# Kernel tuning notes

Measured on AMD Instinct MI355X. Metric: run time of the kernel, lower is better.

## Reference

```python
import jax, jax.numpy as jnp
import numpy as np

C = 1024          # channels
RED = 16          # reduction
RC = C // RED     # 64 bottleneck channels
BZ, NUM_PROPS = 4, 256
BP = BZ * NUM_PROPS


def setup_inputs() -> dict:
    key = jax.random.key(0)
    ks = jax.random.split(key, 10)
    x_props = jax.random.normal(ks[0], (BP, C, 7, 7), dtype=jnp.float32)
    x_query = jax.random.normal(ks[1], (BZ, C, 8, 8), dtype=jnp.float32)
    s_conv = 1.0 / np.sqrt(C)   # kaiming-uniform-ish for conv1d 1x1 (fan_in=C)
    s_mlp = 1.0 / np.sqrt(RC)   # Linear fan_in = RC
    pc_w = jax.random.uniform(ks[2], (RC, C), minval=-s_conv, maxval=s_conv)
    pc_b = jax.random.uniform(ks[3], (RC,), minval=-s_conv, maxval=s_conv)
    qc_w = jax.random.uniform(ks[4], (RC, C), minval=-s_conv, maxval=s_conv)
    qc_b = jax.random.uniform(ks[5], (RC,), minval=-s_conv, maxval=s_conv)
    pm_w = jax.random.uniform(ks[6], (C, RC), minval=-s_mlp, maxval=s_mlp)
    pm_b = jax.random.uniform(ks[7], (C,), minval=-s_mlp, maxval=s_mlp)
    qm_w = jax.random.uniform(ks[8], (C, RC), minval=-s_mlp, maxval=s_mlp)
    qm_b = jax.random.uniform(ks[9], (C,), minval=-s_mlp, maxval=s_mlp)
    return {"x_props": x_props, "x_query": x_query,
            "pc_w": pc_w, "pc_b": pc_b, "qc_w": qc_w, "qc_b": qc_b,
            "pm_w": pm_w, "pm_b": pm_b, "qm_w": qm_w, "qm_b": qm_b}


def reference(x_props, x_query, pc_w, pc_b, qc_w, qc_b, pm_w, pm_b, qm_w, qm_b):
    bp, c, hp, wp = x_props.shape
    bz, _, hq, wq = x_query.shape
    n = bp // bz
    L = hp * wp
    # bilinear resize (half-pixel centers == torch align_corners=False)
    r_query = jax.image.resize(x_query, (bz, c, hp, wp), method='bilinear')
    # 1x1 conv bottlenecks (conv1d over flattened spatial dim)
    q_feat = jnp.einsum('rc,bcl->brl', qc_w, r_query.reshape(bz, c, L)) + qc_b[None, :, None]   # [bz, RC, L]
    p_feat = jnp.einsum('rc,bcl->brl', pc_w, x_props.reshape(bp, c, L)) + pc_b[None, :, None]   # [bp, RC, L]
    # similarity contracts spatial dim; query feature shared across props of same image
    p_feat_g = p_feat.reshape(bz, n, -1, L)
    sim = jnp.einsum('bnrl,bsl->bnrs', p_feat_g, q_feat)                                        # [bz, n, RC, RC]
    p_rel = sim.mean(axis=3).reshape(bp, -1)                                                    # [bp, RC]
    q_rel = sim.mean(axis=2).reshape(bp, -1)                                                    # [bp, RC]
    # channel-gate MLPs
    p_att = jax.nn.sigmoid(p_rel @ pm_w.T + pm_b)                                               # [bp, C]
    q_att = jax.nn.sigmoid(q_rel @ qm_w.T + qm_b)                                               # [bp, C]
    # co-excitation
    f_props = x_props * p_att[:, :, None, None]
    xq_rep = jnp.broadcast_to(x_query[:, None], (bz, n, c, hq, wq)).reshape(bp, c, hq, wq)
    f_query = xq_rep * q_att[:, :, None, None]
    return f_props, f_query, p_att.reshape(bp, c, 1, 1)
```

## Files before the change

### kernel.cpp

```cpp
#include <hip/hip_runtime.h>


typedef float v4f __attribute__((ext_vector_type(4)));

#define WQBAR  0
#define WPCBW  320
#define WPCBB  1344
#define WQF    1408
#define WPMBF  14336
#define WQMBF  47104

#define OUT_FP 0
#define OUT_FQ 51380224
#define OUT_PA 118489088

__device__ __forceinline__ float sigmoidf(float v) {
    return 1.0f / (1.0f + __expf(-v));
}
__device__ __forceinline__ unsigned short bf16_rne(float x) {
    unsigned u = __float_as_uint(x);
    return (unsigned short)((u + 0x7FFFu + ((u >> 16) & 1u)) >> 16);
}
__device__ __forceinline__ unsigned div49(unsigned e) {
    return __umulhi(e, 2804876602u) >> 5;
}

__global__ __launch_bounds__(1024) void k_prepall(
    const float* __restrict__ xq, const float* __restrict__ qc_w,
    const float* __restrict__ qc_b, const float* __restrict__ pc_w,
    const float* __restrict__ pc_b, const float* __restrict__ pm_w,
    const float* __restrict__ qm_w, float* __restrict__ ws)
{
    const int blk = blockIdx.x, t = threadIdx.x;
    if (blk < 196) {
        __shared__ float rq[1024];
        __shared__ float qf_s[64];
        const int b = blk / 49, l = blk - b * 49;
        const int wave = t >> 6, lane = t & 63;
        const int i = l / 7, j = l - i * 7;
        float fi = (2 * i + 1) * (1.0f / 14.0f);
        float fj = (2 * j + 1) * (1.0f / 14.0f);
        float wi0 = (1.0f - 0.875f * fi) * (1.0f / 1.125f); float wi1 = 1.0f - wi0;
        float wj0 = (1.0f - 0.875f * fj) * (1.0f / 1.125f); float wj1 = 1.0f - wj0;
        const float* X = xq + ((size_t)(b * 1024 + t) << 6);
        rq[t] = wi0 * (wj0 * X[i * 8 + j]       + wj1 * X[i * 8 + j + 1])
              + wi1 * (wj0 * X[(i + 1) * 8 + j] + wj1 * X[(i + 1) * 8 + j + 1]);
        __syncthreads();
        #pragma unroll
        for (int ii = 0; ii < 4; ++ii) {
            int s = wave * 4 + ii;
            const float* wr = qc_w + s * 1024;
            float part = 0.0f;
            #pragma unroll
            for (int k = 0; k < 16; ++k) part += wr[k * 64 + lane] * rq[k * 64 + lane];
            #pragma unroll
            for (int off = 32; off; off >>= 1) part += __shfl_down(part, off, 64);
            if (lane == 0) {
                float val = part + qc_b[s];
                ws[WQF + b * 3136 + s * 49 + l] = val;
                qf_s[s] = val;
            }
        }
        __syncthreads();
        if (t == 0) {
            float s = 0.0f;
            #pragma unroll
            for (int k = 0; k < 64; ++k) s += qf_s[k];
            ws[WQBAR + b * 49 + l] = s * (1.0f / 64.0f);
        }
    } else if (blk == 196) {
        float s = 0.0f;
        for (int r = 0; r < 64; ++r) s += pc_w[r * 1024 + t];
        ws[WPCBW + t] = s * (1.0f / 64.0f);
        if (t == 0) {
            float sb = 0.0f;
            for (int r = 0; r < 64; ++r) sb += pc_b[r];
            ws[WPCBB] = sb * (1.0f / 64.0f);
        }
    } else {
        int idx = (blk - 197) * 1024 + t;
        int r = (idx & 65535) >> 10, c = idx & 1023;
        float w = (idx < 65536) ? pm_w[c * 64 + r] : qm_w[c * 64 + r];
        unsigned short* dst = (unsigned short*)(ws + (idx < 65536 ? WPMBF : WQMBF));
        dst[idx & 65535] = bf16_rne(w);
    }
}

__global__ __launch_bounds__(256) void k_red(
    const float* __restrict__ x, const float* __restrict__ xq,
    const float* __restrict__ pc_w, const float* __restrict__ pc_b,
    const float* __restrict__ pm_b, const float* __restrict__ qm_b,
    float* __restrict__ ws, float* __restrict__ patt_out,
    float* __restrict__ fquery)
{
    __shared__ float xs[6272];
    __shared__ float y_s[1024];
    __shared__ float pcb_s[1024];
    __shared__ float qbar_s[49];
    __shared__ float sq_s;
    __shared__ float pbar_part[2][49];
    __shared__ float pbar_s[49];
    __shared__ float prel_s[64];
    __shared__ float qrel_s[64];

    const int t = threadIdx.x, wave = t >> 6, lane = t & 63;
    const int p = blockIdx.x, b = p >> 8;

    if (t < 49) qbar_s[t] = ws[WQBAR + b * 49 + t];
    for (int k = t; k < 1024; k += 256) pcb_s[k] = ws[WPCBW + k];
    const float pcbarb = ws[WPCBB];

    const float4* xp4 = (const float4*)(x + (size_t)p * 50176);
    float pbar_acc = 0.0f;

    for (int ch = 0; ch < 8; ++ch) {
        __syncthreads();
        const float4* src = xp4 + ch * 1568;
        float4* xs4 = (float4*)xs;
        for (int k = t; k < 1568; k += 256) xs4[k] = src[k];
        __syncthreads();
        if (ch == 0 && t == 0) {
            float s = 0.0f;
            #pragma unroll
            for (int l = 0; l < 49; ++l) s += qbar_s[l];
            sq_s = s;
        }
        if (wave < 2) {
            int c = wave * 64 + lane;
            const float* row = xs + c * 49;
            float acc = 0.0f;
            #pragma unroll
            for (int l = 0; l < 49; ++l) acc += row[l] * qbar_s[l];
            y_s[ch * 128 + c] = acc;
        } else if (lane < 49) {
            int cw = (wave - 2) * 64;
            const float* base = xs + cw * 49 + lane;
            const float* pw = pcb_s + ch * 128 + cw;
            float a = 0.0f;
            #pragma unroll
            for (int c = 0; c < 64; ++c) a += pw[c] * base[c * 49];
            pbar_acc += a;
        }
    }
    if (wave >= 2 && lane < 49) pbar_part[wave - 2][lane] = pbar_acc;
    __syncthreads();
    if (t < 49) pbar_s[t] = pbar_part[0][t] + pbar_part[1][t] + pcbarb;
    __syncthreads();
    const float sumqbar = sq_s;

    #pragma unroll
    for (int i = 0; i < 16; ++i) {
        int r = wave * 16 + i;
        const float* wr = pc_w + r * 1024;
        float part = 0.0f;
        #pragma unroll
        for (int k = 0; k < 16; ++k) part += wr[k * 64 + lane] * y_s[k * 64 + lane];
        #pragma unroll
        for (int off = 32; off; off >>= 1) part += __shfl_down(part, off, 64);
        if (lane == 0) prel_s[r] = part + pc_b[r] * sumqbar;
    }
    if (t < 64) {
        const float* qfr = ws + WQF + (b * 3136 + t * 49);
        float a = 0.0f;
        #pragma unroll
        for (int l = 0; l < 49; ++l) a += pbar_s[l] * qfr[l];
        qrel_s[t] = a;
    }
    __syncthreads();

    {
        const unsigned* wp = (const unsigned*)(ws + WPMBF);
        const unsigned* wq = (const unsigned*)(ws + WQMBF);
        float4 ap = {0, 0, 0, 0}, aq = {0, 0, 0, 0};
        #pragma unroll
        for (int r = 0; r < 64; ++r) {
            float pr = prel_s[r], qr = qrel_s[r];
            unsigned p01 = wp[r * 512 + 2 * t];
            unsigned p23 = wp[r * 512 + 2 * t + 1];
            ap.x += __uint_as_float(p01 << 16) * pr;
            ap.y += __uint_as_float(p01 & 0xFFFF0000u) * pr;
            ap.z += __uint_as_float(p23 << 16) * pr;
            ap.w += __uint_as_float(p23 & 0xFFFF0000u) * pr;
            unsigned q01 = wq[r * 512 + 2 * t];
            unsigned q23 = wq[r * 512 + 2 * t + 1];
            aq.x += __uint_as_float(q01 << 16) * qr;
            aq.y += __uint_as_float(q01 & 0xFFFF0000u) * qr;
            aq.z += __uint_as_float(q23 << 16) * qr;
            aq.w += __uint_as_float(q23 & 0xFFFF0000u) * qr;
        }
        float4 pb = ((const float4*)pm_b)[t];
        float4 qb = ((const float4*)qm_b)[t];
        float4 po, qo;
        po.x = sigmoidf(ap.x + pb.x); po.y = sigmoidf(ap.y + pb.y);
        po.z = sigmoidf(ap.z + pb.z); po.w = sigmoidf(ap.w + pb.w);
        qo.x = sigmoidf(aq.x + qb.x); qo.y = sigmoidf(aq.y + qb.y);
        qo.z = sigmoidf(aq.z + qb.z); qo.w = sigmoidf(aq.w + qb.w);
        ((float4*)patt_out)[p * 256 + t] = po;
        ((float4*)pcb_s)[t] = qo;
    }
    __syncthreads();

    const v4f* xq4 = (const v4f*)(xq + ((size_t)b << 16));
    v4f* fq4 = (v4f*)(fquery + ((size_t)p << 16));
    #pragma unroll
    for (int i = 0; i < 64; ++i) {
        int k = i * 256 + t;
        float att = pcb_s[k >> 4];
        v4f v = xq4[k];
        __builtin_nontemporal_store(v * att, fq4 + k);
    }
}

__global__ __launch_bounds__(256) void k_scale(
    const float* __restrict__ x, const float* __restrict__ patt,
    float* __restrict__ fprops)
{
    const unsigned N4 = 12845056u;
    const unsigned stride = gridDim.x * blockDim.x;
    for (unsigned i = blockIdx.x * blockDim.x + threadIdx.x; i < N4; i += stride) {
        unsigned e = i * 4u;
        unsigned q = div49(e);
        unsigned m = e - 49u * q;
        float a0 = patt[q];
        float a1 = patt[q + (m >= 46u)];
        v4f v = ((const v4f*)x)[i];
        v4f g;
        g.x = a0;
        g.y = (m >= 48u) ? a1 : a0;
        g.z = (m >= 47u) ? a1 : a0;
        g.w = (m >= 46u) ? a1 : a0;
        __builtin_nontemporal_store(v * g, (v4f*)fprops + i);
    }
}

extern "C" void kernel_launch(void* const* d_in, const int* in_sizes, int n_in,
                              void* d_out, int out_size, void* d_ws, size_t ws_size,
                              hipStream_t stream) {
    const float* x_props = (const float*)d_in[0];
    const float* x_query = (const float*)d_in[1];
    const float* pc_w    = (const float*)d_in[2];
    const float* pc_b    = (const float*)d_in[3];
    const float* qc_w    = (const float*)d_in[4];
    const float* qc_b    = (const float*)d_in[5];
    const float* pm_w    = (const float*)d_in[6];
    const float* pm_b    = (const float*)d_in[7];
    const float* qm_w    = (const float*)d_in[8];
    const float* qm_b    = (const float*)d_in[9];
    float* out = (float*)d_out;
    float* ws  = (float*)d_ws;

    k_prepall<<<325, 1024, 0, stream>>>(x_query, qc_w, qc_b, pc_w, pc_b, pm_w, qm_w, ws);
    k_red<<<1024, 256, 0, stream>>>(x_props, x_query, pc_w, pc_b, pm_b, qm_b, ws,
                                    out + OUT_PA, out + OUT_FQ);
    k_scale<<<4096, 256, 0, stream>>>(x_props, out + OUT_PA, out + OUT_FP);
}
```

Measured before the change: 168.0 us.

## Fuse proposal scaling into per-proposal reduction kernel to reuse x_props

```diff
diff --git a/kernel.cpp b/kernel.cpp
--- a/kernel.cpp
+++ b/kernel.cpp
@@ -86,12 +86,12 @@
     }
 }
 
-__global__ __launch_bounds__(256) void k_red(
+__global__ __launch_bounds__(256) void k_main(
     const float* __restrict__ x, const float* __restrict__ xq,
     const float* __restrict__ pc_w, const float* __restrict__ pc_b,
     const float* __restrict__ pm_b, const float* __restrict__ qm_b,
     float* __restrict__ ws, float* __restrict__ patt_out,
-    float* __restrict__ fquery)
+    float* __restrict__ fprops, float* __restrict__ fquery)
 {
     __shared__ float xs[6272];
     __shared__ float y_s[1024];
@@ -196,40 +196,41 @@
         qo.x = sigmoidf(aq.x + qb.x); qo.y = sigmoidf(aq.y + qb.y);
         qo.z = sigmoidf(aq.z + qb.z); qo.w = sigmoidf(aq.w + qb.w);
         ((float4*)patt_out)[p * 256 + t] = po;
+        __syncthreads();
+        ((float4*)y_s)[t]   = po;
         ((float4*)pcb_s)[t] = qo;
     }
     __syncthreads();
 
-    const v4f* xq4 = (const v4f*)(xq + ((size_t)b << 16));
-    v4f* fq4 = (v4f*)(fquery + ((size_t)p << 16));
-    #pragma unroll
-    for (int i = 0; i < 64; ++i) {
-        int k = i * 256 + t;
-        float att = pcb_s[k >> 4];
-        v4f v = xq4[k];
-        __builtin_nontemporal_store(v * att, fq4 + k);
-    }
-}
-
-__global__ __launch_bounds__(256) void k_scale(
-    const float* __restrict__ x, const float* __restrict__ patt,
-    float* __restrict__ fprops)
-{
-    const unsigned N4 = 12845056u;
-    const unsigned stride = gridDim.x * blockDim.x;
-    for (unsigned i = blockIdx.x * blockDim.x + threadIdx.x; i < N4; i += stride) {
-        unsigned e = i * 4u;
-        unsigned q = div49(e);
-        unsigned m = e - 49u * q;
-        float a0 = patt[q];
-        float a1 = patt[q + (m >= 46u)];
-        v4f v = ((const v4f*)x)[i];
-        v4f g;
-        g.x = a0;
-        g.y = (m >= 48u) ? a1 : a0;
-        g.z = (m >= 47u) ? a1 : a0;
-        g.w = (m >= 46u) ? a1 : a0;
-        __builtin_nontemporal_store(v * g, (v4f*)fprops + i);
+    {
+        const v4f* xg4 = (const v4f*)(x + (size_t)p * 50176);
+        v4f* fp4 = (v4f*)(fprops + (size_t)p * 50176);
+        for (int i = 0; i < 49; ++i) {
+            int k = i * 256 + t;
+            unsigned e = 4u * (unsigned)k;
+            unsigned c0 = div49(e);
+            unsigned m = e - 49u * c0;
+            float a0 = y_s[c0];
+            float a1 = y_s[c0 + (m >= 46u)];
+            v4f v = xg4[k];
+            v4f g;
+            g.x = a0;
+            g.y = (m >= 48u) ? a1 : a0;
+            g.z = (m >= 47u) ? a1 : a0;
+            g.w = (m >= 46u) ? a1 : a0;
+            __builtin_nontemporal_store(v * g, fp4 + k);
+        }
+    }
+
+    {
+        const v4f* xq4 = (const v4f*)(xq + ((size_t)b << 16));
+        v4f* fq4 = (v4f*)(fquery + ((size_t)p << 16));
+        for (int i = 0; i < 64; ++i) {
+            int k = i * 256 + t;
+            float att = pcb_s[k >> 4];
+            v4f v = xq4[k];
+            __builtin_nontemporal_store(v * att, fq4 + k);
+        }
     }
 }
 
@@ -250,7 +251,6 @@
     float* ws  = (float*)d_ws;
 
     k_prepall<<<325, 1024, 0, stream>>>(x_query, qc_w, qc_b, pc_w, pc_b, pm_w, qm_w, ws);
-    k_red<<<1024, 256, 0, stream>>>(x_props, x_query, pc_w, pc_b, pm_b, qm_b, ws,
-                                    out + OUT_PA, out + OUT_FQ);
-    k_scale<<<4096, 256, 0, stream>>>(x_props, out + OUT_PA, out + OUT_FP);
-}
+    k_main<<<1024, 256, 0, stream>>>(x_props, x_query, pc_w, pc_b, pm_b, qm_b, ws,
+                                     out + OUT_PA, out + OUT_FP, out + OUT_FQ);
+}
```

Result: faster. 160.1 us (-4.7%).
